# Kernel tuning notes

Hardware: AMD Instinct MI355X
Metric: run time of the kernel (lower is better)

Reference implementation:

```python
import jax, jax.numpy as jnp
import numpy as np

B, S, E, H = 4, 2048, 512, 8
DK = E // H
LN_EPS = 1e-5


def setup_inputs() -> dict:
    key = jax.random.key(0)
    ks = jax.random.split(key, 12)
    s_in = 1.0 / np.sqrt(E)
    inp = {
        "Q": jax.random.normal(ks[0], (B, S, E), jnp.float32),
        "K": jax.random.normal(ks[1], (B, S, E), jnp.float32),
        "V": jax.random.normal(ks[2], (B, S, E), jnp.float32),
        # per-head projection weights stacked over heads: [H, E, DK]
        "Wq": jax.random.normal(ks[3], (H, E, DK), jnp.float32) * s_in,
        "bq": jnp.zeros((H, DK), jnp.float32),
        "Wk": jax.random.normal(ks[4], (H, E, DK), jnp.float32) * s_in,
        "bk": jnp.zeros((H, DK), jnp.float32),
        "Wv": jax.random.normal(ks[5], (H, E, DK), jnp.float32) * s_in,
        "bv": jnp.zeros((H, DK), jnp.float32),
        # final linear: [E, E]
        "Wf": jax.random.normal(ks[6], (E, E), jnp.float32) * s_in,
        "bf": jnp.zeros((E,), jnp.float32),
        "gamma": jnp.ones((E,), jnp.float32),
        "beta": jnp.zeros((E,), jnp.float32),
    }
    return inp


def reference(Q, K, V, Wq, bq, Wk, bk, Wv, bv, Wf, bf, gamma, beta):
    scale = DK ** (-0.5)
    # batched per-head projections: [B,H,S,DK]
    q = jnp.einsum("bse,hed->bhsd", Q, Wq) + bq[None, :, None, :]
    k = jnp.einsum("bse,hed->bhsd", K, Wk) + bk[None, :, None, :]
    v = jnp.einsum("bse,hed->bhsd", V, Wv) + bv[None, :, None, :]
    # full QK^T scores [B,H,S,S], scaled, softmax over key axis (dim=2 of bmm == last)
    scores = jnp.einsum("bhsd,bhtd->bhst", q, k) * scale
    attn = jax.nn.softmax(scores, axis=-1)
    ctx = jnp.einsum("bhst,bhtd->bhsd", attn, v)
    # concat heads along feature dim -> [B,S,E]
    z = jnp.transpose(ctx, (0, 2, 1, 3)).reshape(B, S, E)
    residual = jnp.einsum("bse,ef->bsf", z, Wf) + bf
    x = Q + residual
    mean = jnp.mean(x, axis=-1, keepdims=True)
    var = jnp.mean(jnp.square(x - mean), axis=-1, keepdims=True)
    out = (x - mean) * jax.lax.rsqrt(var + LN_EPS) * gamma + beta
    return out
```

## Files before the change

### kernel.cpp

```cpp
#include <hip/hip_runtime.h>
#include <hip/hip_bf16.h>

#define Bb 4
#define Ss 2048
#define Ee 512
#define Hh 8
#define DKk 64

typedef __bf16 bf16_t;
typedef bf16_t bf16x8 __attribute__((ext_vector_type(8)));
typedef bf16_t bf16x4 __attribute__((ext_vector_type(4)));
typedef float f32x4 __attribute__((ext_vector_type(4)));
typedef float f32x16 __attribute__((ext_vector_type(16)));

#define MFMA16(a, b, c) __builtin_amdgcn_mfma_f32_16x16x32_bf16(a, b, c, 0, 0, 0)
#define MFMA32(a, b, c) __builtin_amdgcn_mfma_f32_32x32x16_bf16(a, b, c, 0, 0, 0)

#define GLOAD16(src, dst)                                          \
  __builtin_amdgcn_global_load_lds(                                \
      (const __attribute__((address_space(1))) void*)(src),        \
      (__attribute__((address_space(3))) void*)(dst), 16, 0, 0)

static __device__ __forceinline__ bf16_t f2bf(float f) { return (bf16_t)f; }

static __device__ __forceinline__ float fast_exp2(float x) {
#if __has_builtin(__builtin_amdgcn_exp2f)
  return __builtin_amdgcn_exp2f(x);
#else
  return exp2f(x);
#endif
}

static __device__ __forceinline__ unsigned cvtpk(float lo, float hi) {
  unsigned r;
  asm("v_cvt_pk_bf16_f32 %0, %1, %2" : "=v"(r) : "v"(lo), "v"(hi));
  return r;
}
static __device__ __forceinline__ void plswap(unsigned& a, unsigned& b) {
  asm("v_permlane32_swap_b32 %0, %1" : "+v"(a), "+v"(b));
}

__global__ __launch_bounds__(256) void cvt_k(const float* __restrict__ Q,
                                             const float* __restrict__ K,
                                             const float* __restrict__ V,
                                             bf16_t* __restrict__ dst) {
  int which = blockIdx.x >> 11;
  int bi = blockIdx.x & 2047;
  const float* src = (which == 0) ? Q : ((which == 1) ? K : V);
  bf16_t* d = dst + (size_t)which * ((size_t)Bb * Ss * Ee);
  size_t idx = ((size_t)bi * 256 + threadIdx.x) * 8;
  float4 a = *(const float4*)(src + idx);
  float4 b = *(const float4*)(src + idx + 4);
  bf16x8 o;
  o[0] = f2bf(a.x); o[1] = f2bf(a.y); o[2] = f2bf(a.z); o[3] = f2bf(a.w);
  o[4] = f2bf(b.x); o[5] = f2bf(b.y); o[6] = f2bf(b.z); o[7] = f2bf(b.w);
  *(bf16x8*)(d + idx) = o;
}

__global__ __launch_bounds__(256) void pack_weights_k(
    const float* __restrict__ Wq, const float* __restrict__ Wk,
    const float* __restrict__ Wv, const float* __restrict__ Wf,
    bf16_t* __restrict__ Wt, bf16_t* __restrict__ Wft) {
  __shared__ float tile[64][65];
  int t = threadIdx.x;
  int y = blockIdx.y;
  const float* sp;
  bf16_t* dp;
  int sR, r0, c0;
  if (y < 24) {
    int mat = y >> 3, h = y & 7;
    const float* W = (mat == 0) ? Wq : ((mat == 1) ? Wk : Wv);
    sp = W + (size_t)h * (Ee * DKk);
    sR = 64;
    dp = Wt + (size_t)mat * (Ee * Ee) + (size_t)(h * 64) * Ee;
    r0 = blockIdx.x * 64;
    c0 = 0;
  } else {
    sp = Wf;
    sR = 512;
    dp = Wft;
    r0 = blockIdx.x * 64;
    c0 = (y - 24) * 64;
  }
  int lr = t >> 2, seg = t & 3;
  const float* sprow = sp + (size_t)(r0 + lr) * sR + c0 + seg * 16;
  float4 f0 = ((const float4*)sprow)[0];
  float4 f1 = ((const float4*)sprow)[1];
  float4 f2 = ((const float4*)sprow)[2];
  float4 f3 = ((const float4*)sprow)[3];
  tile[lr][seg * 16 + 0] = f0.x;  tile[lr][seg * 16 + 1] = f0.y;
  tile[lr][seg * 16 + 2] = f0.z;  tile[lr][seg * 16 + 3] = f0.w;
  tile[lr][seg * 16 + 4] = f1.x;  tile[lr][seg * 16 + 5] = f1.y;
  tile[lr][seg * 16 + 6] = f1.z;  tile[lr][seg * 16 + 7] = f1.w;
  tile[lr][seg * 16 + 8] = f2.x;  tile[lr][seg * 16 + 9] = f2.y;
  tile[lr][seg * 16 + 10] = f2.z; tile[lr][seg * 16 + 11] = f2.w;
  tile[lr][seg * 16 + 12] = f3.x; tile[lr][seg * 16 + 13] = f3.y;
  tile[lr][seg * 16 + 14] = f3.z; tile[lr][seg * 16 + 15] = f3.w;
  __syncthreads();
  bf16x8 o0, o1;
#pragma unroll
  for (int i = 0; i < 8; i++) {
    o0[i] = f2bf(tile[seg * 16 + i][lr]);
    o1[i] = f2bf(tile[seg * 16 + 8 + i][lr]);
  }
  bf16_t* dst = dp + (size_t)(c0 + lr) * Ee + r0 + seg * 16;
  *(bf16x8*)dst = o0;
  *(bf16x8*)(dst + 8) = o1;
}

__global__ __launch_bounds__(256) void proj_gemm_k(
    const bf16_t* __restrict__ Xb3, const bf16_t* __restrict__ Wt,
    const float* __restrict__ bq, const float* __restrict__ bk,
    const float* __restrict__ bv, bf16_t* __restrict__ qkv) {
  __shared__ bf16_t As[128 * 64];
  __shared__ bf16_t Bs[128 * 64];
  const int t = threadIdx.x;
  const int zb = blockIdx.z;
  const bf16_t* Ap = Wt + (size_t)zb * (Ee * Ee);
  const bf16_t* Bp = Xb3 + (size_t)zb * ((size_t)Bb * Ss * Ee);
  const float* bias = (zb == 0) ? bq : ((zb == 1) ? bk : bv);
  bf16_t* Outp = qkv + (size_t)zb * ((size_t)Bb * Hh * Ss * DKk);
  const float scl = (zb == 0) ? 0.18033688f : 1.0f;
  const int n0 = blockIdx.x * 128;
  const int m0 = blockIdx.y * 128;
  const int lane = t & 63, w = t >> 6;
  const int wn = w >> 1, wm = w & 1;
  const int rsel = lane & 15, grp = lane >> 4;
  const int wbase = (t & ~63);

  f32x4 acc[4][4];
#pragma unroll
  for (int ni = 0; ni < 4; ni++)
#pragma unroll
    for (int mi = 0; mi < 4; mi++) acc[ni][mi] = (f32x4){0.f, 0.f, 0.f, 0.f};

  for (int k0 = 0; k0 < Ee; k0 += 64) {
#pragma unroll
    for (int i = 0; i < 4; i++) {
      int slot = i * 256 + t;
      int row = slot >> 3;
      int g = (slot & 7) ^ (row & 7);
      GLOAD16(Ap + (size_t)(n0 + row) * Ee + k0 + g * 8,
              As + (size_t)(i * 256 + wbase) * 8);
      GLOAD16(Bp + (size_t)(m0 + row) * Ee + k0 + g * 8,
              Bs + (size_t)(i * 256 + wbase) * 8);
    }
    __syncthreads();
#pragma unroll
    for (int kk = 0; kk < 2; kk++) {
      bf16x8 af[4], bff[4];
#pragma unroll
      for (int ni = 0; ni < 4; ni++) {
        int arow = wn * 64 + ni * 16 + rsel;
        int c = ((kk * 4 + grp) ^ (arow & 7)) * 8;
        af[ni] = *(const bf16x8*)&As[arow * 64 + c];
      }
#pragma unroll
      for (int mi = 0; mi < 4; mi++) {
        int brow = wm * 64 + mi * 16 + rsel;
        int c = ((kk * 4 + grp) ^ (brow & 7)) * 8;
        bff[mi] = *(const bf16x8*)&Bs[brow * 64 + c];
      }
#pragma unroll
      for (int ni = 0; ni < 4; ni++)
#pragma unroll
        for (int mi = 0; mi < 4; mi++)
          acc[ni][mi] = MFMA16(af[ni], bff[mi], acc[ni][mi]);
    }
    __syncthreads();
  }

#pragma unroll
  for (int ni = 0; ni < 4; ni++) {
    int nb = n0 + wn * 64 + ni * 16 + grp * 4;
    float4 b4 = *(const float4*)(bias + nb);
    const float* b4p = (const float*)&b4;
    int hh = nb >> 6, dd = nb & 63;
#pragma unroll
    for (int mi = 0; mi < 4; mi++) {
      int m = m0 + wm * 64 + mi * 16 + rsel;
      int bI = m >> 11, sI = m & 2047;
      bf16x4 o;
#pragma unroll
      for (int r = 0; r < 4; r++)
        o[r] = f2bf((acc[ni][mi][r] + b4p[r]) * scl);
      *(bf16x4*)(Outp + (((size_t)(bI * Hh + hh)) * Ss + sI) * DKk + dd) = o;
    }
  }
}

__global__ __launch_bounds__(256) void final_gemm_k(
    const bf16_t* __restrict__ zin, const bf16_t* __restrict__ Wft,
    const float* __restrict__ bfb, const float* __restrict__ Qres,
    float* __restrict__ x) {
  __shared__ bf16_t As[128 * 64];
  __shared__ bf16_t Bs[128 * 64];
  const int t = threadIdx.x;
  const int n0 = blockIdx.x * 128;
  const int m0 = blockIdx.y * 128;
  const int lane = t & 63, w = t >> 6;
  const int wn = w >> 1, wm = w & 1;
  const int rsel = lane & 15, grp = lane >> 4;
  const int wbase = (t & ~63);

  f32x4 acc[4][4];
#pragma unroll
  for (int ni = 0; ni < 4; ni++)
#pragma unroll
    for (int mi = 0; mi < 4; mi++) acc[ni][mi] = (f32x4){0.f, 0.f, 0.f, 0.f};

  for (int k0 = 0; k0 < Ee; k0 += 64) {
#pragma unroll
    for (int i = 0; i < 4; i++) {
      int slot = i * 256 + t;
      int row = slot >> 3;
      int g = (slot & 7) ^ (row & 7);
      GLOAD16(Wft + (size_t)(n0 + row) * Ee + k0 + g * 8,
              As + (size_t)(i * 256 + wbase) * 8);
      GLOAD16(zin + (size_t)(m0 + row) * Ee + k0 + g * 8,
              Bs + (size_t)(i * 256 + wbase) * 8);
    }
    __syncthreads();
#pragma unroll
    for (int kk = 0; kk < 2; kk++) {
      bf16x8 af[4], bff[4];
#pragma unroll
      for (int ni = 0; ni < 4; ni++) {
        int arow = wn * 64 + ni * 16 + rsel;
        int c = ((kk * 4 + grp) ^ (arow & 7)) * 8;
        af[ni] = *(const bf16x8*)&As[arow * 64 + c];
      }
#pragma unroll
      for (int mi = 0; mi < 4; mi++) {
        int brow = wm * 64 + mi * 16 + rsel;
        int c = ((kk * 4 + grp) ^ (brow & 7)) * 8;
        bff[mi] = *(const bf16x8*)&Bs[brow * 64 + c];
      }
#pragma unroll
      for (int ni = 0; ni < 4; ni++)
#pragma unroll
        for (int mi = 0; mi < 4; mi++)
          acc[ni][mi] = MFMA16(af[ni], bff[mi], acc[ni][mi]);
    }
    __syncthreads();
  }

#pragma unroll
  for (int ni = 0; ni < 4; ni++) {
    int nb = n0 + wn * 64 + ni * 16 + grp * 4;
    float4 b4 = *(const float4*)(bfb + nb);
#pragma unroll
    for (int mi = 0; mi < 4; mi++) {
      int m = m0 + wm * 64 + mi * 16 + rsel;
      float4 q4 = *(const float4*)(Qres + (size_t)m * Ee + nb);
      float4 o;
      o.x = acc[ni][mi][0] + b4.x + q4.x;
      o.y = acc[ni][mi][1] + b4.y + q4.y;
      o.z = acc[ni][mi][2] + b4.z + q4.z;
      o.w = acc[ni][mi][3] + b4.w + q4.w;
      *(float4*)(x + (size_t)m * Ee + nb) = o;
    }
  }
}

__global__ __launch_bounds__(512) void attn_k(const bf16_t* __restrict__ qkv,
                                              bf16_t* __restrict__ zout) {
  const size_t HS = (size_t)Bb * Hh * Ss * DKk;
  __shared__ bf16_t Ks[2][64][68];
  __shared__ bf16_t Vt[2][64][68];
  const int t = threadIdx.x, w = t >> 6, lane = t & 63;
  const int ql = lane & 31, hi = lane >> 5;
  const int bh = blockIdx.y;
  const bf16_t* qp = qkv + (size_t)bh * (Ss * DKk);
  const bf16_t* kp = qp + HS;
  const bf16_t* vp = qp + 2 * HS;
  const int qrow = blockIdx.x * 256 + w * 32 + ql;

  bf16x8 qf0 = *(const bf16x8*)(qp + (size_t)qrow * DKk + 0 + hi * 8);
  bf16x8 qf1 = *(const bf16x8*)(qp + (size_t)qrow * DKk + 16 + hi * 8);
  bf16x8 qf2 = *(const bf16x8*)(qp + (size_t)qrow * DKk + 32 + hi * 8);
  bf16x8 qf3 = *(const bf16x8*)(qp + (size_t)qrow * DKk + 48 + hi * 8);

  const int krow = t >> 3, kch = t & 7;
  const int vkey = t & 63, vdg = w;

  f32x16 ctx0, ctx1;
#pragma unroll
  for (int r = 0; r < 16; r++) { ctx0[r] = 0.f; ctx1[r] = 0.f; }
  float m_run = -1e30f, l_run = 0.f;

  bf16x8 kreg = *(const bf16x8*)(kp + (size_t)krow * DKk + kch * 8);
  bf16x8 vreg = *(const bf16x8*)(vp + (size_t)vkey * DKk + vdg * 8);
  *(bf16x4*)&Ks[0][krow][kch * 8] = __builtin_shufflevector(kreg, kreg, 0, 1, 2, 3);
  *(bf16x4*)&Ks[0][krow][kch * 8 + 4] = __builtin_shufflevector(kreg, kreg, 4, 5, 6, 7);
#pragma unroll
  for (int e = 0; e < 8; e++) Vt[0][vdg * 8 + e][vkey] = vreg[e];
  __syncthreads();

  for (int it = 0; it < Ss / 64; ++it) {
    const int cb = it & 1;
    if (it < Ss / 64 - 1) {
      const size_t off = (size_t)(it + 1) * 64 * DKk;
      kreg = *(const bf16x8*)(kp + off + (size_t)krow * DKk + kch * 8);
      vreg = *(const bf16x8*)(vp + off + (size_t)vkey * DKk + vdg * 8);
    }

    f32x16 st0, st1;
#pragma unroll
    for (int r = 0; r < 16; r++) { st0[r] = 0.f; st1[r] = 0.f; }
#pragma unroll
    for (int s = 0; s < 4; s++) {
      bf16x4 a0 = *(const bf16x4*)&Ks[cb][ql][s * 16 + hi * 8];
      bf16x4 a1 = *(const bf16x4*)&Ks[cb][ql][s * 16 + hi * 8 + 4];
      bf16x8 af = __builtin_shufflevector(a0, a1, 0, 1, 2, 3, 4, 5, 6, 7);
      bf16x4 c0 = *(const bf16x4*)&Ks[cb][32 + ql][s * 16 + hi * 8];
      bf16x4 c1 = *(const bf16x4*)&Ks[cb][32 + ql][s * 16 + hi * 8 + 4];
      bf16x8 af2 = __builtin_shufflevector(c0, c1, 0, 1, 2, 3, 4, 5, 6, 7);
      bf16x8 qf = (s == 0) ? qf0 : ((s == 1) ? qf1 : ((s == 2) ? qf2 : qf3));
      st0 = MFMA32(af, qf, st0);
      st1 = MFMA32(af2, qf, st1);
    }

    float mx = st0[0];
#pragma unroll
    for (int r = 1; r < 16; r++) mx = fmaxf(mx, st0[r]);
#pragma unroll
    for (int r = 0; r < 16; r++) mx = fmaxf(mx, st1[r]);
    mx = fmaxf(mx, __shfl_xor(mx, 32));
    if (__any(mx > m_run + 8.0f)) {
      float mn = fmaxf(m_run, mx);
      float sc = fast_exp2(m_run - mn);
      l_run *= sc;
#pragma unroll
      for (int r = 0; r < 16; r++) { ctx0[r] *= sc; ctx1[r] *= sc; }
      m_run = mn;
    }
    float p0[16], p1[16];
    float ps = 0.f;
#pragma unroll
    for (int r = 0; r < 16; r++) { p0[r] = fast_exp2(st0[r] - m_run); ps += p0[r]; }
#pragma unroll
    for (int r = 0; r < 16; r++) { p1[r] = fast_exp2(st1[r] - m_run); ps += p1[r]; }
    ps += __shfl_xor(ps, 32);
    l_run += ps;

    union U { unsigned u[4]; bf16x8 v; };
    U F00, F01, F10, F11;
    {
      unsigned x0 = cvtpk(p0[0], p0[1]), y0 = cvtpk(p0[4], p0[5]); plswap(x0, y0);
      unsigned x1 = cvtpk(p0[2], p0[3]), y1 = cvtpk(p0[6], p0[7]); plswap(x1, y1);
      F00.u[0] = x0; F00.u[1] = x1; F00.u[2] = y0; F00.u[3] = y1;
      unsigned x2 = cvtpk(p0[8], p0[9]), y2 = cvtpk(p0[12], p0[13]); plswap(x2, y2);
      unsigned x3 = cvtpk(p0[10], p0[11]), y3 = cvtpk(p0[14], p0[15]); plswap(x3, y3);
      F01.u[0] = x2; F01.u[1] = x3; F01.u[2] = y2; F01.u[3] = y3;
      unsigned x4 = cvtpk(p1[0], p1[1]), y4 = cvtpk(p1[4], p1[5]); plswap(x4, y4);
      unsigned x5 = cvtpk(p1[2], p1[3]), y5 = cvtpk(p1[6], p1[7]); plswap(x5, y5);
      F10.u[0] = x4; F10.u[1] = x5; F10.u[2] = y4; F10.u[3] = y5;
      unsigned x6 = cvtpk(p1[8], p1[9]), y6 = cvtpk(p1[12], p1[13]); plswap(x6, y6);
      unsigned x7 = cvtpk(p1[10], p1[11]), y7 = cvtpk(p1[14], p1[15]); plswap(x7, y7);
      F11.u[0] = x6; F11.u[1] = x7; F11.u[2] = y6; F11.u[3] = y7;
    }

    auto rdv = [&](int mtrow, int col) -> bf16x8 {
      bf16x4 lo4 = *(const bf16x4*)&Vt[cb][mtrow + ql][col + hi * 8];
      bf16x4 hi4 = *(const bf16x4*)&Vt[cb][mtrow + ql][col + hi * 8 + 4];
      return __builtin_shufflevector(lo4, hi4, 0, 1, 2, 3, 4, 5, 6, 7);
    };
    ctx0 = MFMA32(rdv(0, 0), F00.v, ctx0);
    ctx0 = MFMA32(rdv(0, 16), F01.v, ctx0);
    ctx0 = MFMA32(rdv(0, 32), F10.v, ctx0);
    ctx0 = MFMA32(rdv(0, 48), F11.v, ctx0);
    ctx1 = MFMA32(rdv(32, 0), F00.v, ctx1);
    ctx1 = MFMA32(rdv(32, 16), F01.v, ctx1);
    ctx1 = MFMA32(rdv(32, 32), F10.v, ctx1);
    ctx1 = MFMA32(rdv(32, 48), F11.v, ctx1);

    if (it < Ss / 64 - 1) {
      *(bf16x4*)&Ks[cb ^ 1][krow][kch * 8] =
          __builtin_shufflevector(kreg, kreg, 0, 1, 2, 3);
      *(bf16x4*)&Ks[cb ^ 1][krow][kch * 8 + 4] =
          __builtin_shufflevector(kreg, kreg, 4, 5, 6, 7);
#pragma unroll
      for (int e = 0; e < 8; e++) Vt[cb ^ 1][vdg * 8 + e][vkey] = vreg[e];
    }
    __syncthreads();
  }

  float inv = 1.f / l_run;
  const int bI = bh >> 3, hh = bh & 7;
  bf16_t* zr = zout + ((size_t)bI * Ss + qrow) * Ee + hh * 64;
#pragma unroll
  for (int a = 0; a < 4; a++) {
    bf16x4 o0, o1;
#pragma unroll
    for (int b2 = 0; b2 < 4; b2++) {
      o0[b2] = f2bf(ctx0[a * 4 + b2] * inv);
      o1[b2] = f2bf(ctx1[a * 4 + b2] * inv);
    }
    *(bf16x4*)(zr + a * 8 + hi * 4) = o0;
    *(bf16x4*)(zr + 32 + a * 8 + hi * 4) = o1;
  }
}

__global__ __launch_bounds__(256) void ln_k(
    const float* __restrict__ x, const float* __restrict__ gamma,
    const float* __restrict__ beta, float* __restrict__ out) {
  int row = blockIdx.x * 4 + (threadIdx.x >> 6);
  int lane = threadIdx.x & 63;
  const float* xr = x + (size_t)row * Ee;
  float4 v0 = *(const float4*)(xr + lane * 8);
  float4 v1 = *(const float4*)(xr + lane * 8 + 4);
  float s = v0.x + v0.y + v0.z + v0.w + v1.x + v1.y + v1.z + v1.w;
  float ss = v0.x * v0.x + v0.y * v0.y + v0.z * v0.z + v0.w * v0.w +
             v1.x * v1.x + v1.y * v1.y + v1.z * v1.z + v1.w * v1.w;
#pragma unroll
  for (int off = 32; off >= 1; off >>= 1) {
    s += __shfl_xor(s, off);
    ss += __shfl_xor(ss, off);
  }
  float mean = s * (1.f / 512.f);
  float var = ss * (1.f / 512.f) - mean * mean;
  float inv = rsqrtf(var + 1e-5f);
  float4 g0 = *(const float4*)(gamma + lane * 8);
  float4 g1 = *(const float4*)(gamma + lane * 8 + 4);
  float4 b0 = *(const float4*)(beta + lane * 8);
  float4 b1 = *(const float4*)(beta + lane * 8 + 4);
  float4 o0, o1;
  o0.x = (v0.x - mean) * inv * g0.x + b0.x;
  o0.y = (v0.y - mean) * inv * g0.y + b0.y;
  o0.z = (v0.z - mean) * inv * g0.z + b0.z;
  o0.w = (v0.w - mean) * inv * g0.w + b0.w;
  o1.x = (v1.x - mean) * inv * g1.x + b1.x;
  o1.y = (v1.y - mean) * inv * g1.y + b1.y;
  o1.z = (v1.z - mean) * inv * g1.z + b1.z;
  o1.w = (v1.w - mean) * inv * g1.w + b1.w;
  float* orow = out + (size_t)row * Ee;
  *(float4*)(orow + lane * 8) = o0;
  *(float4*)(orow + lane * 8 + 4) = o1;
}

extern "C" void kernel_launch(void* const* d_in, const int* in_sizes, int n_in,
                              void* d_out, int out_size, void* d_ws, size_t ws_size,
                              hipStream_t stream) {
  const float* Q = (const float*)d_in[0];
  const float* K = (const float*)d_in[1];
  const float* V = (const float*)d_in[2];
  const float* Wq = (const float*)d_in[3];
  const float* bq = (const float*)d_in[4];
  const float* Wk = (const float*)d_in[5];
  const float* bk = (const float*)d_in[6];
  const float* Wv = (const float*)d_in[7];
  const float* bv = (const float*)d_in[8];
  const float* Wf = (const float*)d_in[9];
  const float* bfb = (const float*)d_in[10];
  const float* gamma = (const float*)d_in[11];
  const float* beta = (const float*)d_in[12];
  float* out = (float*)d_out;

  bf16_t* Wt = (bf16_t*)d_ws;
  bf16_t* Wft = Wt + 3 * Ee * Ee;
  bf16_t* qkv = Wft + Ee * Ee;
  bf16_t* sA = qkv + (size_t)3 * Bb * Hh * Ss * DKk;
  bf16_t* z = sA;
  float* x = (float*)qkv;

  cvt_k<<<dim3(6144), dim3(256), 0, stream>>>(Q, K, V, sA);
  pack_weights_k<<<dim3(8, 32), dim3(256), 0, stream>>>(Wq, Wk, Wv, Wf, Wt, Wft);
  proj_gemm_k<<<dim3(4, 64, 3), dim3(256), 0, stream>>>(sA, Wt, bq, bk, bv, qkv);
  attn_k<<<dim3(8, 32), dim3(512), 0, stream>>>(qkv, z);
  final_gemm_k<<<dim3(4, 64), dim3(256), 0, stream>>>(z, Wft, bfb, Q, x);
  ln_k<<<dim3(2048), dim3(256), 0, stream>>>(x, gamma, beta, out);
}
```

Baseline: 211.2 us.

## Split attention keys across wave halves, pre-transpose V, swizzle GEMM tile order

Result: no change. 208.0 us (-1.6%).

```diff
diff --git a/kernel.cpp b/kernel.cpp
--- a/kernel.cpp
+++ b/kernel.cpp
@@ -20,6 +20,9 @@
   __builtin_amdgcn_global_load_lds(                                \
       (const __attribute__((address_space(1))) void*)(src),        \
       (__attribute__((address_space(3))) void*)(dst), 16, 0, 0)
+
+#define LO4(v) __builtin_shufflevector(v, v, 0, 1, 2, 3)
+#define HI4(v) __builtin_shufflevector(v, v, 4, 5, 6, 7)
 
 static __device__ __forceinline__ bf16_t f2bf(float f) { return (bf16_t)f; }
 
@@ -108,6 +111,32 @@
   *(bf16x8*)(dst + 8) = o1;
 }
 
+__global__ __launch_bounds__(256) void vt_k(const bf16_t* __restrict__ vsrc,
+                                            bf16_t* __restrict__ vtG) {
+  __shared__ bf16_t tile[64][68];
+  const int t = threadIdx.x;
+  const int bh = blockIdx.y;
+  const int s0 = blockIdx.x * 64;
+  const bf16_t* vp = vsrc + (size_t)bh * (Ss * DKk);
+  const int r = t >> 2, seg = t & 3;
+  const bf16_t* src = vp + (size_t)(s0 + r) * DKk + seg * 16;
+  bf16x8 a = ((const bf16x8*)src)[0];
+  bf16x8 b = ((const bf16x8*)src)[1];
+  bf16_t* ld = &tile[r][seg * 16];
+  *(bf16x4*)(ld + 0) = LO4(a); *(bf16x4*)(ld + 4) = HI4(a);
+  *(bf16x4*)(ld + 8) = LO4(b); *(bf16x4*)(ld + 12) = HI4(b);
+  __syncthreads();
+  bf16x8 o0, o1;
+#pragma unroll
+  for (int j = 0; j < 8; j++) {
+    o0[j] = tile[seg * 16 + j][r];
+    o1[j] = tile[seg * 16 + 8 + j][r];
+  }
+  bf16_t* dst = vtG + (size_t)bh * ((size_t)DKk * Ss) + (size_t)r * Ss + s0 + seg * 16;
+  *(bf16x8*)dst = o0;
+  *(bf16x8*)(dst + 8) = o1;
+}
+
 __global__ __launch_bounds__(256) void proj_gemm_k(
     const bf16_t* __restrict__ Xb3, const bf16_t* __restrict__ Wt,
     const float* __restrict__ bq, const float* __restrict__ bk,
@@ -121,8 +150,10 @@
   const float* bias = (zb == 0) ? bq : ((zb == 1) ? bk : bv);
   bf16_t* Outp = qkv + (size_t)zb * ((size_t)Bb * Hh * Ss * DKk);
   const float scl = (zb == 0) ? 0.18033688f : 1.0f;
-  const int n0 = blockIdx.x * 128;
-  const int m0 = blockIdx.y * 128;
+  const int id = blockIdx.x + (blockIdx.y << 2);
+  const int nid = (id & 7) * 32 + (id >> 3);
+  const int n0 = (nid & 3) * 128;
+  const int m0 = (nid >> 2) * 128;
   const int lane = t & 63, w = t >> 6;
   const int wn = w >> 1, wm = w & 1;
   const int rsel = lane & 15, grp = lane >> 4;
@@ -196,8 +227,10 @@
   __shared__ bf16_t As[128 * 64];
   __shared__ bf16_t Bs[128 * 64];
   const int t = threadIdx.x;
-  const int n0 = blockIdx.x * 128;
-  const int m0 = blockIdx.y * 128;
+  const int id = blockIdx.x + (blockIdx.y << 2);
+  const int nid = (id & 7) * 32 + (id >> 3);
+  const int n0 = (nid & 3) * 128;
+  const int m0 = (nid >> 2) * 128;
   const int lane = t & 63, w = t >> 6;
   const int wn = w >> 1, wm = w & 1;
   const int rsel = lane & 15, grp = lane >> 4;
@@ -263,63 +296,79 @@
   }
 }
 
-__global__ __launch_bounds__(512) void attn_k(const bf16_t* __restrict__ qkv,
-                                              bf16_t* __restrict__ zout) {
+__global__ __launch_bounds__(512, 4) void attn_k(const bf16_t* __restrict__ qkv,
+                                                 const bf16_t* __restrict__ vtG,
+                                                 bf16_t* __restrict__ zout) {
   const size_t HS = (size_t)Bb * Hh * Ss * DKk;
-  __shared__ bf16_t Ks[2][64][68];
-  __shared__ bf16_t Vt[2][64][68];
+  __shared__ __align__(16) unsigned char smem_raw[2 * 34816];
+  bf16_t (*Ks)[2][64][68] = reinterpret_cast<bf16_t (*)[2][64][68]>(smem_raw);
+  bf16_t (*Vt)[2][64][68] = reinterpret_cast<bf16_t (*)[2][64][68]>(smem_raw + 34816);
   const int t = threadIdx.x, w = t >> 6, lane = t & 63;
+  const int qsub = w >> 1, half = w & 1;
   const int ql = lane & 31, hi = lane >> 5;
   const int bh = blockIdx.y;
   const bf16_t* qp = qkv + (size_t)bh * (Ss * DKk);
   const bf16_t* kp = qp + HS;
-  const bf16_t* vp = qp + 2 * HS;
-  const int qrow = blockIdx.x * 256 + w * 32 + ql;
+  const bf16_t* vt = vtG + (size_t)bh * ((size_t)DKk * Ss);
+  const int qrow = blockIdx.x * 128 + qsub * 32 + ql;
 
   bf16x8 qf0 = *(const bf16x8*)(qp + (size_t)qrow * DKk + 0 + hi * 8);
   bf16x8 qf1 = *(const bf16x8*)(qp + (size_t)qrow * DKk + 16 + hi * 8);
   bf16x8 qf2 = *(const bf16x8*)(qp + (size_t)qrow * DKk + 32 + hi * 8);
   bf16x8 qf3 = *(const bf16x8*)(qp + (size_t)qrow * DKk + 48 + hi * 8);
 
-  const int krow = t >> 3, kch = t & 7;
-  const int vkey = t & 63, vdg = w;
+  const int sid = qsub * 64 + lane;
+  const int srow = sid >> 2, sseg = sid & 3;
+  const int koff0 = half * (Ss / 2);
 
   f32x16 ctx0, ctx1;
 #pragma unroll
   for (int r = 0; r < 16; r++) { ctx0[r] = 0.f; ctx1[r] = 0.f; }
   float m_run = -1e30f, l_run = 0.f;
 
-  bf16x8 kreg = *(const bf16x8*)(kp + (size_t)krow * DKk + kch * 8);
-  bf16x8 vreg = *(const bf16x8*)(vp + (size_t)vkey * DKk + vdg * 8);
-  *(bf16x4*)&Ks[0][krow][kch * 8] = __builtin_shufflevector(kreg, kreg, 0, 1, 2, 3);
-  *(bf16x4*)&Ks[0][krow][kch * 8 + 4] = __builtin_shufflevector(kreg, kreg, 4, 5, 6, 7);
-#pragma unroll
-  for (int e = 0; e < 8; e++) Vt[0][vdg * 8 + e][vkey] = vreg[e];
+  {
+    const bf16_t* ksrc = kp + (size_t)(koff0 + srow) * DKk + sseg * 16;
+    bf16x8 ka = ((const bf16x8*)ksrc)[0], kb = ((const bf16x8*)ksrc)[1];
+    const bf16_t* vsrc = vt + (size_t)srow * Ss + koff0 + sseg * 16;
+    bf16x8 va = ((const bf16x8*)vsrc)[0], vb = ((const bf16x8*)vsrc)[1];
+    bf16_t* kd = &Ks[half][0][srow][sseg * 16];
+    *(bf16x4*)(kd + 0) = LO4(ka); *(bf16x4*)(kd + 4) = HI4(ka);
+    *(bf16x4*)(kd + 8) = LO4(kb); *(bf16x4*)(kd + 12) = HI4(kb);
+    bf16_t* vd = &Vt[half][0][srow][sseg * 16];
+    *(bf16x4*)(vd + 0) = LO4(va); *(bf16x4*)(vd + 4) = HI4(va);
+    *(bf16x4*)(vd + 8) = LO4(vb); *(bf16x4*)(vd + 12) = HI4(vb);
+  }
   __syncthreads();
 
-  for (int it = 0; it < Ss / 64; ++it) {
+  const int NT = (Ss / 2) / 64;
+  bf16x8 pk0, pk1, pv0, pv1;
+  for (int it = 0; it < NT; ++it) {
     const int cb = it & 1;
-    if (it < Ss / 64 - 1) {
-      const size_t off = (size_t)(it + 1) * 64 * DKk;
-      kreg = *(const bf16x8*)(kp + off + (size_t)krow * DKk + kch * 8);
-      vreg = *(const bf16x8*)(vp + off + (size_t)vkey * DKk + vdg * 8);
+    if (it < NT - 1) {
+      const int k0 = koff0 + (it + 1) * 64;
+      const bf16_t* ksrc = kp + (size_t)(k0 + srow) * DKk + sseg * 16;
+      pk0 = ((const bf16x8*)ksrc)[0]; pk1 = ((const bf16x8*)ksrc)[1];
+      const bf16_t* vsrc = vt + (size_t)srow * Ss + k0 + sseg * 16;
+      pv0 = ((const bf16x8*)vsrc)[0]; pv1 = ((const bf16x8*)vsrc)[1];
     }
 
     f32x16 st0, st1;
 #pragma unroll
     for (int r = 0; r < 16; r++) { st0[r] = 0.f; st1[r] = 0.f; }
+    __builtin_amdgcn_s_setprio(1);
 #pragma unroll
     for (int s = 0; s < 4; s++) {
-      bf16x4 a0 = *(const bf16x4*)&Ks[cb][ql][s * 16 + hi * 8];
-      bf16x4 a1 = *(const bf16x4*)&Ks[cb][ql][s * 16 + hi * 8 + 4];
+      bf16x4 a0 = *(const bf16x4*)&Ks[half][cb][ql][s * 16 + hi * 8];
+      bf16x4 a1 = *(const bf16x4*)&Ks[half][cb][ql][s * 16 + hi * 8 + 4];
       bf16x8 af = __builtin_shufflevector(a0, a1, 0, 1, 2, 3, 4, 5, 6, 7);
-      bf16x4 c0 = *(const bf16x4*)&Ks[cb][32 + ql][s * 16 + hi * 8];
-      bf16x4 c1 = *(const bf16x4*)&Ks[cb][32 + ql][s * 16 + hi * 8 + 4];
+      bf16x4 c0 = *(const bf16x4*)&Ks[half][cb][32 + ql][s * 16 + hi * 8];
+      bf16x4 c1 = *(const bf16x4*)&Ks[half][cb][32 + ql][s * 16 + hi * 8 + 4];
       bf16x8 af2 = __builtin_shufflevector(c0, c1, 0, 1, 2, 3, 4, 5, 6, 7);
       bf16x8 qf = (s == 0) ? qf0 : ((s == 1) ? qf1 : ((s == 2) ? qf2 : qf3));
       st0 = MFMA32(af, qf, st0);
       st1 = MFMA32(af2, qf, st1);
     }
+    __builtin_amdgcn_s_setprio(0);
 
     float mx = st0[0];
 #pragma unroll
@@ -335,37 +384,37 @@
       for (int r = 0; r < 16; r++) { ctx0[r] *= sc; ctx1[r] *= sc; }
       m_run = mn;
     }
-    float p0[16], p1[16];
     float ps = 0.f;
 #pragma unroll
-    for (int r = 0; r < 16; r++) { p0[r] = fast_exp2(st0[r] - m_run); ps += p0[r]; }
-#pragma unroll
-    for (int r = 0; r < 16; r++) { p1[r] = fast_exp2(st1[r] - m_run); ps += p1[r]; }
+    for (int r = 0; r < 16; r++) { st0[r] = fast_exp2(st0[r] - m_run); ps += st0[r]; }
+#pragma unroll
+    for (int r = 0; r < 16; r++) { st1[r] = fast_exp2(st1[r] - m_run); ps += st1[r]; }
     ps += __shfl_xor(ps, 32);
     l_run += ps;
 
     union U { unsigned u[4]; bf16x8 v; };
     U F00, F01, F10, F11;
     {
-      unsigned x0 = cvtpk(p0[0], p0[1]), y0 = cvtpk(p0[4], p0[5]); plswap(x0, y0);
-      unsigned x1 = cvtpk(p0[2], p0[3]), y1 = cvtpk(p0[6], p0[7]); plswap(x1, y1);
+      unsigned x0 = cvtpk(st0[0], st0[1]), y0 = cvtpk(st0[4], st0[5]); plswap(x0, y0);
+      unsigned x1 = cvtpk(st0[2], st0[3]), y1 = cvtpk(st0[6], st0[7]); plswap(x1, y1);
       F00.u[0] = x0; F00.u[1] = x1; F00.u[2] = y0; F00.u[3] = y1;
-      unsigned x2 = cvtpk(p0[8], p0[9]), y2 = cvtpk(p0[12], p0[13]); plswap(x2, y2);
-      unsigned x3 = cvtpk(p0[10], p0[11]), y3 = cvtpk(p0[14], p0[15]); plswap(x3, y3);
+      unsigned x2 = cvtpk(st0[8], st0[9]), y2 = cvtpk(st0[12], st0[13]); plswap(x2, y2);
+      unsigned x3 = cvtpk(st0[10], st0[11]), y3 = cvtpk(st0[14], st0[15]); plswap(x3, y3);
       F01.u[0] = x2; F01.u[1] = x3; F01.u[2] = y2; F01.u[3] = y3;
-      unsigned x4 = cvtpk(p1[0], p1[1]), y4 = cvtpk(p1[4], p1[5]); plswap(x4, y4);
-      unsigned x5 = cvtpk(p1[2], p1[3]), y5 = cvtpk(p1[6], p1[7]); plswap(x5, y5);
+      unsigned x4 = cvtpk(st1[0], st1[1]), y4 = cvtpk(st1[4], st1[5]); plswap(x4, y4);
+      unsigned x5 = cvtpk(st1[2], st1[3]), y5 = cvtpk(st1[6], st1[7]); plswap(x5, y5);
       F10.u[0] = x4; F10.u[1] = x5; F10.u[2] = y4; F10.u[3] = y5;
-      unsigned x6 = cvtpk(p1[8], p1[9]), y6 = cvtpk(p1[12], p1[13]); plswap(x6, y6);
-      unsigned x7 = cvtpk(p1[10], p1[11]), y7 = cvtpk(p1[14], p1[15]); plswap(x7, y7);
+      unsigned x6 = cvtpk(st1[8], st1[9]), y6 = cvtpk(st1[12], st1[13]); plswap(x6, y6);
+      unsigned x7 = cvtpk(st1[10], st1[11]), y7 = cvtpk(st1[14], st1[15]); plswap(x7, y7);
       F11.u[0] = x6; F11.u[1] = x7; F11.u[2] = y6; F11.u[3] = y7;
     }
 
     auto rdv = [&](int mtrow, int col) -> bf16x8 {
-      bf16x4 lo4 = *(const bf16x4*)&Vt[cb][mtrow + ql][col + hi * 8];
-      bf16x4 hi4 = *(const bf16x4*)&Vt[cb][mtrow + ql][col + hi * 8 + 4];
+      bf16x4 lo4 = *(const bf16x4*)&Vt[half][cb][mtrow + ql][col + hi * 8];
+      bf16x4 hi4 = *(const bf16x4*)&Vt[half][cb][mtrow + ql][col + hi * 8 + 4];
       return __builtin_shufflevector(lo4, hi4, 0, 1, 2, 3, 4, 5, 6, 7);
     };
+    __builtin_amdgcn_s_setprio(1);
     ctx0 = MFMA32(rdv(0, 0), F00.v, ctx0);
     ctx0 = MFMA32(rdv(0, 16), F01.v, ctx0);
     ctx0 = MFMA32(rdv(0, 32), F10.v, ctx0);
@@ -374,31 +423,49 @@
     ctx1 = MFMA32(rdv(32, 16), F01.v, ctx1);
     ctx1 = MFMA32(rdv(32, 32), F10.v, ctx1);
     ctx1 = MFMA32(rdv(32, 48), F11.v, ctx1);
-
-    if (it < Ss / 64 - 1) {
-      *(bf16x4*)&Ks[cb ^ 1][krow][kch * 8] =
-          __builtin_shufflevector(kreg, kreg, 0, 1, 2, 3);
-      *(bf16x4*)&Ks[cb ^ 1][krow][kch * 8 + 4] =
-          __builtin_shufflevector(kreg, kreg, 4, 5, 6, 7);
-#pragma unroll
-      for (int e = 0; e < 8; e++) Vt[cb ^ 1][vdg * 8 + e][vkey] = vreg[e];
+    __builtin_amdgcn_s_setprio(0);
+
+    if (it < NT - 1) {
+      bf16_t* kd = &Ks[half][cb ^ 1][srow][sseg * 16];
+      *(bf16x4*)(kd + 0) = LO4(pk0); *(bf16x4*)(kd + 4) = HI4(pk0);
+      *(bf16x4*)(kd + 8) = LO4(pk1); *(bf16x4*)(kd + 12) = HI4(pk1);
+      bf16_t* vd = &Vt[half][cb ^ 1][srow][sseg * 16];
+      *(bf16x4*)(vd + 0) = LO4(pv0); *(bf16x4*)(vd + 4) = HI4(pv0);
+      *(bf16x4*)(vd + 8) = LO4(pv1); *(bf16x4*)(vd + 12) = HI4(pv1);
     }
     __syncthreads();
   }
 
-  float inv = 1.f / l_run;
-  const int bI = bh >> 3, hh = bh & 7;
-  bf16_t* zr = zout + ((size_t)bI * Ss + qrow) * Ee + hh * 64;
-#pragma unroll
-  for (int a = 0; a < 4; a++) {
-    bf16x4 o0, o1;
-#pragma unroll
-    for (int b2 = 0; b2 < 4; b2++) {
-      o0[b2] = f2bf(ctx0[a * 4 + b2] * inv);
-      o1[b2] = f2bf(ctx1[a * 4 + b2] * inv);
-    }
-    *(bf16x4*)(zr + a * 8 + hi * 4) = o0;
-    *(bf16x4*)(zr + 32 + a * 8 + hi * 4) = o1;
+  float* mr = (float*)smem_raw;
+  const int msl = qsub * 64 + lane;
+  float* cslot = mr + msl * 33;
+  float* mym = mr + 8448;
+  float* myl = mr + 8704;
+  if (half == 1) {
+#pragma unroll
+    for (int r = 0; r < 16; r++) { cslot[r] = ctx0[r]; cslot[16 + r] = ctx1[r]; }
+    mym[msl] = m_run;
+    myl[msl] = l_run;
+  }
+  __syncthreads();
+  if (half == 0) {
+    float m1 = mym[msl], l1 = myl[msl];
+    float mt = fmaxf(m_run, m1);
+    float f0 = fast_exp2(m_run - mt), f1 = fast_exp2(m1 - mt);
+    float inv = 1.f / (l_run * f0 + l1 * f1);
+    const int bI = bh >> 3, hh = bh & 7;
+    bf16_t* zr = zout + ((size_t)bI * Ss + qrow) * Ee + hh * 64;
+#pragma unroll
+    for (int a = 0; a < 4; a++) {
+      bf16x4 o0, o1;
+#pragma unroll
+      for (int b2 = 0; b2 < 4; b2++) {
+        o0[b2] = f2bf((ctx0[a * 4 + b2] * f0 + cslot[a * 4 + b2] * f1) * inv);
+        o1[b2] = f2bf((ctx1[a * 4 + b2] * f0 + cslot[16 + a * 4 + b2] * f1) * inv);
+      }
+      *(bf16x4*)(zr + a * 8 + hi * 4) = o0;
+      *(bf16x4*)(zr + 32 + a * 8 + hi * 4) = o1;
+    }
   }
 }
 
@@ -462,12 +529,14 @@
   bf16_t* qkv = Wft + Ee * Ee;
   bf16_t* sA = qkv + (size_t)3 * Bb * Hh * Ss * DKk;
   bf16_t* z = sA;
+  bf16_t* vtG = sA + (size_t)Bb * Hh * Ss * DKk;
   float* x = (float*)qkv;
 
   cvt_k<<<dim3(6144), dim3(256), 0, stream>>>(Q, K, V, sA);
   pack_weights_k<<<dim3(8, 32), dim3(256), 0, stream>>>(Wq, Wk, Wv, Wf, Wt, Wft);
   proj_gemm_k<<<dim3(4, 64, 3), dim3(256), 0, stream>>>(sA, Wt, bq, bk, bv, qkv);
-  attn_k<<<dim3(8, 32), dim3(512), 0, stream>>>(qkv, z);
+  vt_k<<<dim3(32, 32), dim3(256), 0, stream>>>(qkv + (size_t)2 * Bb * Hh * Ss * DKk, vtG);
+  attn_k<<<dim3(16, 32), dim3(512), 0, stream>>>(qkv, vtG, z);
   final_gemm_k<<<dim3(4, 64), dim3(256), 0, stream>>>(z, Wft, bfb, Q, x);
   ln_k<<<dim3(2048), dim3(256), 0, stream>>>(x, gamma, beta, out);
 }
```
